# Kernel optimization log

Measured on AMD Instinct MI355X. Metric: run time of the kernel, lower is better.

The kernel has to match this reference:

```python
import jax, jax.numpy as jnp
import numpy as np

D = 128       # d_model
NHEAD = 4
R = 2         # n_rounds
CF = 32       # fine channels
H0, W0 = 40, 52
HF, WF = 160, 208
TEMP = 0.1
THR = 0.2
WIN = 5
STRIDE = 8


def setup_inputs() -> dict:
    key = jax.random.key(0)
    ks = jax.random.split(key, 24)
    s = 0.05
    f = jnp.float32
    n = lambda k, sh: jax.random.normal(k, sh, f)
    inp = {
        'coarse0': n(ks[0], (1, D, H0, W0)),
        'coarse1': n(ks[1], (1, D, H0, W0)),
        'fine0': n(ks[2], (1, CF, HF, WF)),
        'fine1': n(ks[3], (1, CF, HF, WF)),
        'sa_in_w': n(ks[4], (R, 3 * D, D)) * s,
        'sa_in_b': jnp.zeros((R, 3 * D), f),
        'sa_out_w': n(ks[5], (R, D, D)) * s,
        'sa_out_b': jnp.zeros((R, D), f),
        'ca_in_w': n(ks[6], (R, 3 * D, D)) * s,
        'ca_in_b': jnp.zeros((R, 3 * D), f),
        'ca_out_w': n(ks[7], (R, D, D)) * s,
        'ca_out_b': jnp.zeros((R, D), f),
        'sn_g': jnp.ones((R, D), f), 'sn_b': jnp.zeros((R, D), f),
        'cn_g': jnp.ones((R, D), f), 'cn_b': jnp.zeros((R, D), f),
        'ffn_w1': n(ks[8], (R, 2 * D, D)) * s,
        'ffn_b1': jnp.zeros((R, 2 * D), f),
        'ffn_w2': n(ks[9], (R, D, 2 * D)) * s,
        'ffn_b2': jnp.zeros((R, D), f),
        'fn_g': jnp.ones((R, D), f), 'fn_b': jnp.zeros((R, D), f),
        'proj_w': n(ks[10], (CF, CF)) * s,
        'proj_b': jnp.zeros((CF,), f),
    }
    return inp


def _ln(x, g, b):
    m = x.mean(-1, keepdims=True)
    v = ((x - m) ** 2).mean(-1, keepdims=True)
    return (x - m) * jax.lax.rsqrt(v + 1e-5) * g + b


def _mha(xq, xkv, in_w, in_b, out_w, out_b):
    B, Lq, d = xq.shape
    Lk = xkv.shape[1]
    h, dh = NHEAD, D // NHEAD
    q = (xq @ in_w[:d].T + in_b[:d]).reshape(B, Lq, h, dh)
    k = (xkv @ in_w[d:2 * d].T + in_b[d:2 * d]).reshape(B, Lk, h, dh)
    v = (xkv @ in_w[2 * d:].T + in_b[2 * d:]).reshape(B, Lk, h, dh)
    a = jnp.einsum('bqhd,bkhd->bhqk', q, k) / np.float32(np.sqrt(dh))
    a = jax.nn.softmax(a, axis=-1)
    o = jnp.einsum('bhqk,bkhd->bqhd', a, v).reshape(B, Lq, d)
    return o @ out_w.T + out_b


def _forward(coarse0, coarse1, fine0, fine1, sa_in_w, sa_in_b, sa_out_w, sa_out_b,
             ca_in_w, ca_in_b, ca_out_w, ca_out_b, sn_g, sn_b, cn_g, cn_b,
             ffn_w1, ffn_b1, ffn_w2, ffn_b2, fn_g, fn_b, proj_w, proj_b):
    B, C, H, W = coarse0.shape
    f0 = coarse0.reshape(B, C, H * W).transpose(0, 2, 1)
    f1 = coarse1.reshape(B, C, H * W).transpose(0, 2, 1)
    for i in range(R):
        f0 = _ln(f0 + _mha(f0, f0, sa_in_w[i], sa_in_b[i], sa_out_w[i], sa_out_b[i]), sn_g[i], sn_b[i])
        f1 = _ln(f1 + _mha(f1, f1, sa_in_w[i], sa_in_b[i], sa_out_w[i], sa_out_b[i]), sn_g[i], sn_b[i])
        f0c = _mha(f0, f1, ca_in_w[i], ca_in_b[i], ca_out_w[i], ca_out_b[i])
        f1c = _mha(f1, f0, ca_in_w[i], ca_in_b[i], ca_out_w[i], ca_out_b[i])
        f0 = _ln(f0 + f0c, cn_g[i], cn_b[i])
        f1 = _ln(f1 + f1c, cn_g[i], cn_b[i])
        f0 = _ln(f0 + jax.nn.relu(f0 @ ffn_w1[i].T + ffn_b1[i]) @ ffn_w2[i].T + ffn_b2[i], fn_g[i], fn_b[i])
        f1 = _ln(f1 + jax.nn.relu(f1 @ ffn_w1[i].T + ffn_b1[i]) @ ffn_w2[i].T + ffn_b2[i], fn_g[i], fn_b[i])
    # coarse matching: dual softmax + mutual NN
    f0n = f0 / jnp.maximum(jnp.linalg.norm(f0, axis=-1, keepdims=True), 1e-12)
    f1n = f1 / jnp.maximum(jnp.linalg.norm(f1, axis=-1, keepdims=True), 1e-12)
    S = jnp.einsum('bld,bmd->blm', f0n, f1n) / TEMP
    P = jax.nn.softmax(S, axis=-1) * jax.nn.softmax(S, axis=-2)
    P0 = P[0]
    L0 = H * W
    idx0 = jnp.argmax(P0, axis=-1)
    idx1 = jnp.argmax(P0, axis=0)
    conf = P0.max(axis=-1)
    valid = (idx1[idx0] == jnp.arange(L0)) & (conf > THR)
    ar = jnp.arange(L0)
    mk0 = jnp.stack([ar % W, ar // W], 1).astype(jnp.float32)
    mk1 = jnp.stack([idx0 % W, idx0 // W], 1).astype(jnp.float32)
    # fine refinement (vectorized over all L0 candidate matches)
    f0p = jnp.einsum('oc,chw->ohw', proj_w, fine0[0]) + proj_b[:, None, None]
    f1p = jnp.einsum('oc,chw->ohw', proj_w, fine1[0]) + proj_b[:, None, None]
    half = WIN // 2
    fr = STRIDE // 2
    c0 = (mk0 * fr).astype(jnp.int32)
    c1 = (mk1 * fr).astype(jnp.int32)
    Hf, Wf = f0p.shape[1], f0p.shape[2]
    inb = ((c0[:, 0] - half >= 0) & (c0[:, 0] + half < Wf) & (c0[:, 1] - half >= 0) & (c0[:, 1] + half < Hf)
           & (c1[:, 0] - half >= 0) & (c1[:, 0] + half < Wf) & (c1[:, 1] - half >= 0) & (c1[:, 1] + half < Hf))
    off = jnp.arange(WIN) - half
    cy0 = jnp.clip(c0[:, 1], half, Hf - 1 - half)
    cx0 = jnp.clip(c0[:, 0], half, Wf - 1 - half)
    cy1 = jnp.clip(c1[:, 1], half, Hf - 1 - half)
    cx1 = jnp.clip(c1[:, 0], half, Wf - 1 - half)
    center = f0p[:, cy0, cx0]                              # (C, N)
    y1 = cy1[:, None] + off
    x1 = cx1[:, None] + off
    patch1 = f1p[:, y1[:, :, None], x1[:, None, :]]
    corr = jnp.einsum('cn,cnhw->nhw', center, patch1)
    soft = jax.nn.softmax(corr.reshape(-1, WIN * WIN), axis=-1).reshape(-1, WIN, WIN)
    gx = off.astype(jnp.float32)[None, None, :]
    gy = off.astype(jnp.float32)[None, :, None]
    offx = (soft * gx).sum((1, 2))
    offy = (soft * gy).sum((1, 2))
    scale = np.float32(STRIDE // fr)
    pt0 = mk0 * STRIDE + STRIDE // 2
    base1 = mk1 * STRIDE + STRIDE // 2
    delta = jnp.stack([offx, offy], 1) * scale
    pt1 = base1 + jnp.where(inb[:, None], delta, 0.0)
    return P, valid, conf, pt0, pt1


def reference(coarse0, coarse1, fine0, fine1, sa_in_w, sa_in_b, sa_out_w, sa_out_b,
              ca_in_w, ca_in_b, ca_out_w, ca_out_b, sn_g, sn_b, cn_g, cn_b,
              ffn_w1, ffn_b1, ffn_w2, ffn_b2, fn_g, fn_b, proj_w, proj_b):
    return _forward(coarse0, coarse1, fine0, fine1, sa_in_w, sa_in_b, sa_out_w, sa_out_b,
                    ca_in_w, ca_in_b, ca_out_w, ca_out_b, sn_g, sn_b, cn_g, cn_b,
                    ffn_w1, ffn_b1, ffn_w2, ffn_b2, fn_g, fn_b, proj_w, proj_b)
```

## Files before the change

### kernel.cpp

```cpp
#include <hip/hip_runtime.h>
#include <math.h>

#define LTOK 2080
#define DIM 128
#define NH 4
#define W0C 52
#define HFI 160
#define WFI 208
#define NPIX (HFI*WFI)
#define CFCH 32
#define NSPLIT2 6
#define QBLK 64
#define NQB 33
#define PSTRIDE2 2112
#define NST 33

#define DOT4(q,k) ((q).x*(k).x + (q).y*(k).y + (q).z*(k).z + (q).w*(k).w)

__global__ __launch_bounds__(256) void transpose_b_kernel(const float* __restrict__ in0,
                                                          const float* __restrict__ in1,
                                                          float* __restrict__ out0,
                                                          float* __restrict__ out1)
{
    const float* in = blockIdx.z ? in1 : in0;
    float* out = blockIdx.z ? out1 : out0;
    __shared__ float T[32][33];
    int l0 = blockIdx.x * 32, c0 = blockIdx.y * 32;
    int t = threadIdx.x;
    #pragma unroll
    for (int e = 0; e < 4; ++e) {
        int idx = t + e * 256; int i = idx >> 5, j = idx & 31;
        T[i][j] = in[(size_t)(c0 + i) * LTOK + l0 + j];
    }
    __syncthreads();
    #pragma unroll
    for (int e = 0; e < 4; ++e) {
        int idx = t + e * 256; int j2 = idx >> 5, i2 = idx & 31;
        out[(size_t)(l0 + j2) * DIM + c0 + i2] = T[i2][j2];
    }
}

__global__ __launch_bounds__(256) void gemm64_nt_b2_kernel(const float* __restrict__ A0,
                                                           const float* __restrict__ A1, int lda,
                                                           const float* __restrict__ B, int ldb,
                                                           float* __restrict__ C0,
                                                           float* __restrict__ C1, int ldc,
                                                           int K,
                                                           const float* __restrict__ bias, int relu,
                                                           int M)
{
    const float* A = blockIdx.z ? A1 : A0;
    float* C = blockIdx.z ? C1 : C0;
    __shared__ float As[32][68];
    __shared__ float Bs[32][68];
    int tid = threadIdx.x;
    int n0 = blockIdx.x * 64, m0 = blockIdx.y * 64;
    int cg = tid & 15, rg = tid >> 4;
    int r0 = rg * 4, c0 = cg * 4;
    int srow = tid & 63;
    int skq  = tid >> 6;
    float4 acc0 = make_float4(0.f,0.f,0.f,0.f);
    float4 acc1 = make_float4(0.f,0.f,0.f,0.f);
    float4 acc2 = make_float4(0.f,0.f,0.f,0.f);
    float4 acc3 = make_float4(0.f,0.f,0.f,0.f);

    for (int k0 = 0; k0 < K; k0 += 32) {
        int ar = m0 + srow; ar = ar < M ? ar : M - 1;
        int br = n0 + srow;
        const float* ap = A + (size_t)ar * lda + k0 + skq * 8;
        const float* bp = B + (size_t)br * ldb + k0 + skq * 8;
        float4 av0 = *(const float4*)(ap);
        float4 av1 = *(const float4*)(ap + 4);
        float4 bv0 = *(const float4*)(bp);
        float4 bv1 = *(const float4*)(bp + 4);
        int kk = skq * 8;
        As[kk+0][srow] = av0.x; As[kk+1][srow] = av0.y; As[kk+2][srow] = av0.z; As[kk+3][srow] = av0.w;
        As[kk+4][srow] = av1.x; As[kk+5][srow] = av1.y; As[kk+6][srow] = av1.z; As[kk+7][srow] = av1.w;
        Bs[kk+0][srow] = bv0.x; Bs[kk+1][srow] = bv0.y; Bs[kk+2][srow] = bv0.z; Bs[kk+3][srow] = bv0.w;
        Bs[kk+4][srow] = bv1.x; Bs[kk+5][srow] = bv1.y; Bs[kk+6][srow] = bv1.z; Bs[kk+7][srow] = bv1.w;
        __syncthreads();
        #pragma unroll
        for (int k = 0; k < 32; ++k) {
            float4 a = *(const float4*)(&As[k][r0]);
            float4 b = *(const float4*)(&Bs[k][c0]);
            acc0.x += a.x*b.x; acc0.y += a.x*b.y; acc0.z += a.x*b.z; acc0.w += a.x*b.w;
            acc1.x += a.y*b.x; acc1.y += a.y*b.y; acc1.z += a.y*b.z; acc1.w += a.y*b.w;
            acc2.x += a.z*b.x; acc2.y += a.z*b.y; acc2.z += a.z*b.z; acc2.w += a.z*b.w;
            acc3.x += a.w*b.x; acc3.y += a.w*b.y; acc3.z += a.w*b.z; acc3.w += a.w*b.w;
        }
        __syncthreads();
    }
    float4 bv = make_float4(0.f,0.f,0.f,0.f);
    if (bias) bv = *(const float4*)(bias + n0 + c0);
    acc0.x += bv.x; acc0.y += bv.y; acc0.z += bv.z; acc0.w += bv.w;
    acc1.x += bv.x; acc1.y += bv.y; acc1.z += bv.z; acc1.w += bv.w;
    acc2.x += bv.x; acc2.y += bv.y; acc2.z += bv.z; acc2.w += bv.w;
    acc3.x += bv.x; acc3.y += bv.y; acc3.z += bv.z; acc3.w += bv.w;
    if (relu) {
        acc0.x = fmaxf(acc0.x, 0.f); acc0.y = fmaxf(acc0.y, 0.f); acc0.z = fmaxf(acc0.z, 0.f); acc0.w = fmaxf(acc0.w, 0.f);
        acc1.x = fmaxf(acc1.x, 0.f); acc1.y = fmaxf(acc1.y, 0.f); acc1.z = fmaxf(acc1.z, 0.f); acc1.w = fmaxf(acc1.w, 0.f);
        acc2.x = fmaxf(acc2.x, 0.f); acc2.y = fmaxf(acc2.y, 0.f); acc2.z = fmaxf(acc2.z, 0.f); acc2.w = fmaxf(acc2.w, 0.f);
        acc3.x = fmaxf(acc3.x, 0.f); acc3.y = fmaxf(acc3.y, 0.f); acc3.z = fmaxf(acc3.z, 0.f); acc3.w = fmaxf(acc3.w, 0.f);
    }
    int gr = m0 + r0;
    if (gr + 0 < M) *(float4*)(C + (size_t)(gr + 0) * ldc + n0 + c0) = acc0;
    if (gr + 1 < M) *(float4*)(C + (size_t)(gr + 1) * ldc + n0 + c0) = acc1;
    if (gr + 2 < M) *(float4*)(C + (size_t)(gr + 2) * ldc + n0 + c0) = acc2;
    if (gr + 3 < M) *(float4*)(C + (size_t)(gr + 3) * ldc + n0 + c0) = acc3;
}

__global__ __launch_bounds__(256) void gemm_score64_kernel(const float* __restrict__ A,
                                                           const float* __restrict__ B,
                                                           float* __restrict__ C,
                                                           float2* __restrict__ prs,
                                                           float2* __restrict__ pcs)
{
    __shared__ float As[32][68];
    __shared__ float Bs[32][68];
    __shared__ float cmS[16][68];
    __shared__ float ceS[16][68];
    int tid = threadIdx.x;
    int n0 = blockIdx.x * 64, m0 = blockIdx.y * 64;
    int cg = tid & 15, rg = tid >> 4;
    int r0 = rg * 4, c0 = cg * 4;
    int srow = tid & 63;
    int skq  = tid >> 6;
    float4 acc0 = make_float4(0.f,0.f,0.f,0.f);
    float4 acc1 = make_float4(0.f,0.f,0.f,0.f);
    float4 acc2 = make_float4(0.f,0.f,0.f,0.f);
    float4 acc3 = make_float4(0.f,0.f,0.f,0.f);

    for (int k0 = 0; k0 < 128; k0 += 32) {
        int ar = m0 + srow; ar = ar < LTOK ? ar : LTOK - 1;
        int br = n0 + srow; br = br < LTOK ? br : LTOK - 1;
        const float* ap = A + (size_t)ar * 128 + k0 + skq * 8;
        const float* bp = B + (size_t)br * 128 + k0 + skq * 8;
        float4 av0 = *(const float4*)(ap);
        float4 av1 = *(const float4*)(ap + 4);
        float4 bv0 = *(const float4*)(bp);
        float4 bv1 = *(const float4*)(bp + 4);
        int kk = skq * 8;
        As[kk+0][srow] = av0.x; As[kk+1][srow] = av0.y; As[kk+2][srow] = av0.z; As[kk+3][srow] = av0.w;
        As[kk+4][srow] = av1.x; As[kk+5][srow] = av1.y; As[kk+6][srow] = av1.z; As[kk+7][srow] = av1.w;
        Bs[kk+0][srow] = bv0.x; Bs[kk+1][srow] = bv0.y; Bs[kk+2][srow] = bv0.z; Bs[kk+3][srow] = bv0.w;
        Bs[kk+4][srow] = bv1.x; Bs[kk+5][srow] = bv1.y; Bs[kk+6][srow] = bv1.z; Bs[kk+7][srow] = bv1.w;
        __syncthreads();
        #pragma unroll
        for (int k = 0; k < 32; ++k) {
            float4 a = *(const float4*)(&As[k][r0]);
            float4 b = *(const float4*)(&Bs[k][c0]);
            acc0.x += a.x*b.x; acc0.y += a.x*b.y; acc0.z += a.x*b.z; acc0.w += a.x*b.w;
            acc1.x += a.y*b.x; acc1.y += a.y*b.y; acc1.z += a.y*b.z; acc1.w += a.y*b.w;
            acc2.x += a.z*b.x; acc2.y += a.z*b.y; acc2.z += a.z*b.z; acc2.w += a.z*b.w;
            acc3.x += a.w*b.x; acc3.y += a.w*b.y; acc3.z += a.w*b.z; acc3.w += a.w*b.w;
        }
        __syncthreads();
    }
    acc0.x *= 10.f; acc0.y *= 10.f; acc0.z *= 10.f; acc0.w *= 10.f;
    acc1.x *= 10.f; acc1.y *= 10.f; acc1.z *= 10.f; acc1.w *= 10.f;
    acc2.x *= 10.f; acc2.y *= 10.f; acc2.z *= 10.f; acc2.w *= 10.f;
    acc3.x *= 10.f; acc3.y *= 10.f; acc3.z *= 10.f; acc3.w *= 10.f;
    int gr = m0 + r0;
    bool colv = (n0 + c0) < LTOK;
    if (colv) {
        if (gr + 0 < LTOK) *(float4*)(C + (size_t)(gr + 0) * LTOK + n0 + c0) = acc0;
        if (gr + 1 < LTOK) *(float4*)(C + (size_t)(gr + 1) * LTOK + n0 + c0) = acc1;
        if (gr + 2 < LTOK) *(float4*)(C + (size_t)(gr + 2) * LTOK + n0 + c0) = acc2;
        if (gr + 3 < LTOK) *(float4*)(C + (size_t)(gr + 3) * LTOK + n0 + c0) = acc3;
    }
    const float NEG = -1e30f;
    float v00 = colv ? acc0.x : NEG, v01 = colv ? acc0.y : NEG, v02 = colv ? acc0.z : NEG, v03 = colv ? acc0.w : NEG;
    float v10 = colv ? acc1.x : NEG, v11 = colv ? acc1.y : NEG, v12 = colv ? acc1.z : NEG, v13 = colv ? acc1.w : NEG;
    float v20 = colv ? acc2.x : NEG, v21 = colv ? acc2.y : NEG, v22 = colv ? acc2.z : NEG, v23 = colv ? acc2.w : NEG;
    float v30 = colv ? acc3.x : NEG, v31 = colv ? acc3.y : NEG, v32 = colv ? acc3.z : NEG, v33 = colv ? acc3.w : NEG;
    #pragma unroll
    for (int i = 0; i < 4; ++i) {
        float a = (i==0)?v00:(i==1)?v10:(i==2)?v20:v30;
        float b = (i==0)?v01:(i==1)?v11:(i==2)?v21:v31;
        float c = (i==0)?v02:(i==1)?v12:(i==2)?v22:v32;
        float d = (i==0)?v03:(i==1)?v13:(i==2)?v23:v33;
        float m = fmaxf(fmaxf(a,b), fmaxf(c,d));
        float e = 0.f;
        if (m > NEG) e = __expf(a-m) + __expf(b-m) + __expf(c-m) + __expf(d-m);
        #pragma unroll
        for (int mm = 8; mm >= 1; mm >>= 1) {
            float m2 = __shfl_xor(m, mm, 16);
            float e2 = __shfl_xor(e, mm, 16);
            if (m2 > m) { e = e * __expf(m - m2) + e2; m = m2; }
            else if (m2 > NEG) { e += e2 * __expf(m2 - m); }
        }
        if (cg == 0 && gr + i < LTOK)
            prs[(size_t)blockIdx.x * LTOK + gr + i] = make_float2(m, e);
    }
    bool rv0 = (gr + 0) < LTOK, rv1 = (gr + 1) < LTOK, rv2 = (gr + 2) < LTOK, rv3 = (gr + 3) < LTOK;
    #pragma unroll
    for (int j = 0; j < 4; ++j) {
        float a = rv0 ? ((j==0)?v00:(j==1)?v01:(j==2)?v02:v03) : NEG;
        float b = rv1 ? ((j==0)?v10:(j==1)?v11:(j==2)?v12:v13) : NEG;
        float c = rv2 ? ((j==0)?v20:(j==1)?v21:(j==2)?v22:v23) : NEG;
        float d = rv3 ? ((j==0)?v30:(j==1)?v31:(j==2)?v32:v33) : NEG;
        float m = fmaxf(fmaxf(a,b), fmaxf(c,d));
        float e = 0.f;
        if (m > NEG) {
            if (rv0) e += __expf(a-m);
            if (rv1) e += __expf(b-m);
            if (rv2) e += __expf(c-m);
            if (rv3) e += __expf(d-m);
        }
        cmS[rg][c0 + j] = m;
        ceS[rg][c0 + j] = e;
    }
    __syncthreads();
    if (tid < 64) {
        int col = tid;
        float m = cmS[0][col], e = ceS[0][col];
        #pragma unroll
        for (int k = 1; k < 16; ++k) {
            float m2 = cmS[k][col], e2 = ceS[k][col];
            if (m2 > m) { e = e * __expf(m - m2) + e2; m = m2; }
            else if (m2 > NEG) { e += e2 * __expf(m2 - m); }
        }
        if (n0 + col < LTOK)
            pcs[(size_t)blockIdx.y * LTOK + n0 + col] = make_float2(m, e);
    }
}

__global__ __launch_bounds__(256) void stats_combine_kernel(const float2* __restrict__ prs,
                                                            const float2* __restrict__ pcs,
                                                            float* __restrict__ rowmax,
                                                            float* __restrict__ rsinv,
                                                            float* __restrict__ colmax,
                                                            float* __restrict__ csinv)
{
    int id = blockIdx.x * 256 + threadIdx.x;
    if (id >= 2 * LTOK) return;
    const float2* p = (id < LTOK) ? (prs + id) : (pcs + (id - LTOK));
    float M = -1e30f;
    for (int i = 0; i < NST; ++i) M = fmaxf(M, p[(size_t)i * LTOK].x);
    float S = 0.f;
    for (int i = 0; i < NST; ++i) {
        float2 f = p[(size_t)i * LTOK];
        S += f.y * __expf(f.x - M);
    }
    if (id < LTOK) { rowmax[id] = M; rsinv[id] = 1.f / S; }
    else           { colmax[id - LTOK] = M; csinv[id - LTOK] = 1.f / S; }
}

__global__ __launch_bounds__(256) void dualp_argmax_kernel(float* __restrict__ S,
                                                           const float* __restrict__ rm,
                                                           const float* __restrict__ rsinv,
                                                           const float* __restrict__ cm,
                                                           const float* __restrict__ csinv,
                                                           float* __restrict__ prv,
                                                           int* __restrict__ pri,
                                                           float* __restrict__ pcv,
                                                           int* __restrict__ pci)
{
    __shared__ float cvS[8][32];
    __shared__ int   ciS[8][32];
    int tid = threadIdx.x;
    int n0 = blockIdx.x * 32, m0 = blockIdx.y * 32;
    int c = tid & 31, r8 = tid >> 5;
    int col = n0 + c;
    float cmv = cm[col], csv = csinv[col];
    float p[4];
    #pragma unroll
    for (int jj = 0; jj < 4; ++jj) {
        int row = m0 + 4 * r8 + jj;
        size_t o = (size_t)row * LTOK + col;
        float s = S[o];
        float pv = __expf(2.f * s - rm[row] - cmv) * (rsinv[row] * csv);
        S[o] = pv;
        p[jj] = pv;
    }
    #pragma unroll
    for (int jj = 0; jj < 4; ++jj) {
        float bv = p[jj]; int bi = col;
        #pragma unroll
        for (int mm = 16; mm >= 1; mm >>= 1) {
            float ov = __shfl_xor(bv, mm, 32);
            int   oi = __shfl_xor(bi, mm, 32);
            if (ov > bv || (ov == bv && oi < bi)) { bv = ov; bi = oi; }
        }
        if (c == 0) {
            prv[(size_t)blockIdx.x * LTOK + m0 + 4 * r8 + jj] = bv;
            pri[(size_t)blockIdx.x * LTOK + m0 + 4 * r8 + jj] = bi;
        }
    }
    float bv = p[0]; int bi = m0 + 4 * r8;
    #pragma unroll
    for (int jj = 1; jj < 4; ++jj)
        if (p[jj] > bv) { bv = p[jj]; bi = m0 + 4 * r8 + jj; }
    cvS[r8][c] = bv; ciS[r8][c] = bi;
    __syncthreads();
    if (r8 == 0) {
        #pragma unroll
        for (int k = 1; k < 8; ++k)
            if (cvS[k][c] > bv) { bv = cvS[k][c]; bi = ciS[k][c]; }
        pcv[(size_t)blockIdx.y * LTOK + col] = bv;
        pci[(size_t)blockIdx.y * LTOK + col] = bi;
    }
}

__global__ __launch_bounds__(256) void argmax_combine_kernel(const float* __restrict__ prv,
                                                             const int* __restrict__ pri,
                                                             const float* __restrict__ pcv,
                                                             const int* __restrict__ pci,
                                                             int* __restrict__ idx0,
                                                             float* __restrict__ conf,
                                                             int* __restrict__ idx1)
{
    int id = blockIdx.x * 256 + threadIdx.x;
    if (id >= 2 * LTOK) return;
    if (id < LTOK) {
        float best = -1e30f; int bi = 0;
        for (int i = 0; i < 65; ++i) {
            float v = prv[(size_t)i * LTOK + id];
            if (v > best) { best = v; bi = pri[(size_t)i * LTOK + id]; }
        }
        idx0[id] = bi; conf[id] = best;
    } else {
        int colI = id - LTOK;
        float best = -1e30f; int bi = 0;
        for (int i = 0; i < 65; ++i) {
            float v = pcv[(size_t)i * LTOK + colI];
            if (v > best) { best = v; bi = pci[(size_t)i * LTOK + colI]; }
        }
        idx1[colI] = bi;
    }
}

__global__ __launch_bounds__(256, 3) void mha_partial2_kernel(const float* __restrict__ qkvA,
                                                              const float* __restrict__ qkvB,
                                                              int cross,
                                                              float* __restrict__ part)
{
    __shared__ float Qs[QBLK][36];
    __shared__ float Ks[64][36];
    __shared__ float Vt[32][68];
    __shared__ float Ps[QBLK][68];
    int tid = threadIdx.x;
    int qb = blockIdx.x, ns = blockIdx.z;
    int img = blockIdx.y >> 2, h = blockIdx.y & 3;
    const float* qsrc  = img ? qkvB : qkvA;
    const float* kvsrc = cross ? (img ? qkvA : qkvB) : qsrc;
    int c4 = tid & 15;
    int rg = tid >> 4;
    const int r0 = rg * 4;
    const float sc = 0.17677669529663687f;

    {
        int r = tid >> 2, d8 = (tid & 3) << 3;
        int qr = qb * QBLK + r; qr = qr < LTOK ? qr : (LTOK - 1);
        const float* src = qsrc + (size_t)qr * 384 + h * 32 + d8;
        *(float4*)(&Qs[r][d8])     = *(const float4*)(src);
        *(float4*)(&Qs[r][d8 + 4]) = *(const float4*)(src + 4);
    }
    float a00=0.f,a01=0.f,a10=0.f,a11=0.f,a20=0.f,a21=0.f,a30=0.f,a31=0.f;
    float l0=0.f,l1=0.f,l2=0.f,l3=0.f;
    __syncthreads();

    const int koff = 128 + h * 32, voff = 256 + h * 32;
    for (int t = ns; t < 33; t += NSPLIT2) {
        int j0 = t * 64;
        {
            int r = tid >> 3, d4 = (tid & 7) << 2;
            int j1 = j0 + r, j2 = j0 + r + 32;
            float4 k1 = *(const float4*)(kvsrc + (size_t)j1 * 384 + koff + d4);
            float4 v1 = *(const float4*)(kvsrc + (size_t)j1 * 384 + voff + d4);
            float4 k2 = make_float4(0.f, 0.f, 0.f, 0.f);
            float4 v2 = make_float4(0.f, 0.f, 0.f, 0.f);
            if (j2 < LTOK) {
                k2 = *(const float4*)(kvsrc + (size_t)j2 * 384 + koff + d4);
                v2 = *(const float4*)(kvsrc + (size_t)j2 * 384 + voff + d4);
            }
            *(float4*)(&Ks[r][d4])      = k1;
            *(float4*)(&Ks[r + 32][d4]) = k2;
            Vt[d4 + 0][r] = v1.x; Vt[d4 + 1][r] = v1.y; Vt[d4 + 2][r] = v1.z; Vt[d4 + 3][r] = v1.w;
            Vt[d4 + 0][r + 32] = v2.x; Vt[d4 + 1][r + 32] = v2.y; Vt[d4 + 2][r + 32] = v2.z; Vt[d4 + 3][r + 32] = v2.w;
        }
        __syncthreads();
        float s00=0.f,s01=0.f,s02=0.f,s03=0.f;
        float s10=0.f,s11=0.f,s12=0.f,s13=0.f;
        float s20=0.f,s21=0.f,s22=0.f,s23=0.f;
        float s30=0.f,s31=0.f,s32=0.f,s33=0.f;
        #pragma unroll
        for (int d4 = 0; d4 < 8; ++d4) {
            const int db = d4 << 2;
            float4 k0 = *(const float4*)(&Ks[c4][db]);
            float4 k1 = *(const float4*)(&Ks[c4 + 16][db]);
            float4 k2 = *(const float4*)(&Ks[c4 + 32][db]);
            float4 k3 = *(const float4*)(&Ks[c4 + 48][db]);
            float4 q0 = *(const float4*)(&Qs[r0 + 0][db]);
            float4 q1 = *(const float4*)(&Qs[r0 + 1][db]);
            float4 q2 = *(const float4*)(&Qs[r0 + 2][db]);
            float4 q3 = *(const float4*)(&Qs[r0 + 3][db]);
            s00 += DOT4(q0,k0); s01 += DOT4(q0,k1); s02 += DOT4(q0,k2); s03 += DOT4(q0,k3);
            s10 += DOT4(q1,k0); s11 += DOT4(q1,k1); s12 += DOT4(q1,k2); s13 += DOT4(q1,k3);
            s20 += DOT4(q2,k0); s21 += DOT4(q2,k1); s22 += DOT4(q2,k2); s23 += DOT4(q2,k3);
            s30 += DOT4(q3,k0); s31 += DOT4(q3,k1); s32 += DOT4(q3,k2); s33 += DOT4(q3,k3);
        }
        bool ok0 = (j0 + c4) < LTOK;
        bool ok1 = (j0 + 16 + c4) < LTOK;
        bool ok2 = (j0 + 32 + c4) < LTOK;
        bool ok3 = (j0 + 48 + c4) < LTOK;
        {
            float p0 = ok0 ? __expf(s00 * sc) : 0.f;
            float p1 = ok1 ? __expf(s01 * sc) : 0.f;
            float p2 = ok2 ? __expf(s02 * sc) : 0.f;
            float p3 = ok3 ? __expf(s03 * sc) : 0.f;
            l0 += p0 + p1 + p2 + p3;
            Ps[r0 + 0][c4] = p0; Ps[r0 + 0][c4 + 16] = p1; Ps[r0 + 0][c4 + 32] = p2; Ps[r0 + 0][c4 + 48] = p3;
        }
        {
            float p0 = ok0 ? __expf(s10 * sc) : 0.f;
            float p1 = ok1 ? __expf(s11 * sc) : 0.f;
            float p2 = ok2 ? __expf(s12 * sc) : 0.f;
            float p3 = ok3 ? __expf(s13 * sc) : 0.f;
            l1 += p0 + p1 + p2 + p3;
            Ps[r0 + 1][c4] = p0; Ps[r0 + 1][c4 + 16] = p1; Ps[r0 + 1][c4 + 32] = p2; Ps[r0 + 1][c4 + 48] = p3;
        }
        {
            float p0 = ok0 ? __expf(s20 * sc) : 0.f;
            float p1 = ok1 ? __expf(s21 * sc) : 0.f;
            float p2 = ok2 ? __expf(s22 * sc) : 0.f;
            float p3 = ok3 ? __expf(s23 * sc) : 0.f;
            l2 += p0 + p1 + p2 + p3;
            Ps[r0 + 2][c4] = p0; Ps[r0 + 2][c4 + 16] = p1; Ps[r0 + 2][c4 + 32] = p2; Ps[r0 + 2][c4 + 48] = p3;
        }
        {
            float p0 = ok0 ? __expf(s30 * sc) : 0.f;
            float p1 = ok1 ? __expf(s31 * sc) : 0.f;
            float p2 = ok2 ? __expf(s32 * sc) : 0.f;
            float p3 = ok3 ? __expf(s33 * sc) : 0.f;
            l3 += p0 + p1 + p2 + p3;
            Ps[r0 + 3][c4] = p0; Ps[r0 + 3][c4 + 16] = p1; Ps[r0 + 3][c4 + 32] = p2; Ps[r0 + 3][c4 + 48] = p3;
        }
        __syncthreads();
        #pragma unroll
        for (int j4 = 0; j4 < 16; ++j4) {
            const int jb = j4 << 2;
            float4 v0 = *(const float4*)(&Vt[c4][jb]);
            float4 v1 = *(const float4*)(&Vt[c4 + 16][jb]);
            float4 pq0 = *(const float4*)(&Ps[r0 + 0][jb]);
            float4 pq1 = *(const float4*)(&Ps[r0 + 1][jb]);
            float4 pq2 = *(const float4*)(&Ps[r0 + 2][jb]);
            float4 pq3 = *(const float4*)(&Ps[r0 + 3][jb]);
            a00 += DOT4(pq0,v0); a01 += DOT4(pq0,v1);
            a10 += DOT4(pq1,v0); a11 += DOT4(pq1,v1);
            a20 += DOT4(pq2,v0); a21 += DOT4(pq2,v1);
            a30 += DOT4(pq3,v0); a31 += DOT4(pq3,v1);
        }
        __syncthreads();
    }
    float* pb = part + (size_t)((((size_t)img * NQB + qb) * NH + h) * NSPLIT2 + ns) * PSTRIDE2;
    pb[(r0 + 0) * 32 + c4]      = a00;
    pb[(r0 + 0) * 32 + c4 + 16] = a01;
    pb[(r0 + 1) * 32 + c4]      = a10;
    pb[(r0 + 1) * 32 + c4 + 16] = a11;
    pb[(r0 + 2) * 32 + c4]      = a20;
    pb[(r0 + 2) * 32 + c4 + 16] = a21;
    pb[(r0 + 3) * 32 + c4]      = a30;
    pb[(r0 + 3) * 32 + c4 + 16] = a31;
    #pragma unroll
    for (int mm = 8; mm >= 1; mm >>= 1) {
        l0 += __shfl_xor(l0, mm, 16);
        l1 += __shfl_xor(l1, mm, 16);
        l2 += __shfl_xor(l2, mm, 16);
        l3 += __shfl_xor(l3, mm, 16);
    }
    if (c4 == 0) {
        pb[2048 + r0 + 0] = l0;
        pb[2048 + r0 + 1] = l1;
        pb[2048 + r0 + 2] = l2;
        pb[2048 + r0 + 3] = l3;
    }
}

__global__ __launch_bounds__(256) void mha_combine2_kernel(const float* __restrict__ part,
                                                           float* __restrict__ out0,
                                                           float* __restrict__ out1)
{
    int tid = threadIdx.x;
    int qb = blockIdx.x;
    int img = blockIdx.y >> 2, h = blockIdx.y & 3;
    float* out = img ? out1 : out0;
    int c = tid & 31, rg8 = tid >> 5;
    const float* pb = part + (size_t)(((size_t)img * NQB + qb) * NH + h) * NSPLIT2 * PSTRIDE2;
    #pragma unroll
    for (int jj = 0; jj < 8; ++jj) {
        int row = rg8 * 8 + jj;
        int qrow = qb * QBLK + row;
        if (qrow >= LTOK) continue;
        float num = 0.f, den = 0.f;
        #pragma unroll
        for (int ns = 0; ns < NSPLIT2; ++ns) {
            num += pb[ns * PSTRIDE2 + row * 32 + c];
            den += pb[ns * PSTRIDE2 + 2048 + row];
        }
        out[(size_t)qrow * DIM + h * 32 + c] = num / den;
    }
}

__global__ __launch_bounds__(256) void addln_b_kernel(float* __restrict__ f0,
                                                      float* __restrict__ f1,
                                                      const float* __restrict__ t0,
                                                      const float* __restrict__ t1,
                                                      const float* __restrict__ g,
                                                      const float* __restrict__ b)
{
    float* f = blockIdx.y ? f1 : f0;
    const float* t = blockIdx.y ? t1 : t0;
    int row = blockIdx.x * 4 + (threadIdx.x >> 6);
    int lane = threadIdx.x & 63;
    size_t base = (size_t)row * DIM;
    float x0 = f[base + lane] + t[base + lane];
    float x1 = f[base + lane + 64] + t[base + lane + 64];
    float s = x0 + x1;
    #pragma unroll
    for (int mm = 32; mm >= 1; mm >>= 1) s += __shfl_xor(s, mm, 64);
    float mean = s * (1.f / 128.f);
    float d0 = x0 - mean, d1 = x1 - mean;
    float v = d0 * d0 + d1 * d1;
    #pragma unroll
    for (int mm = 32; mm >= 1; mm >>= 1) v += __shfl_xor(v, mm, 64);
    float rstd = rsqrtf(v * (1.f / 128.f) + 1e-5f);
    f[base + lane]      = d0 * rstd * g[lane] + b[lane];
    f[base + lane + 64] = d1 * rstd * g[lane + 64] + b[lane + 64];
}

__global__ __launch_bounds__(256) void normrows_b_kernel(const float* __restrict__ i0,
                                                         const float* __restrict__ i1,
                                                         float* __restrict__ o0,
                                                         float* __restrict__ o1)
{
    const float* f = blockIdx.y ? i1 : i0;
    float* o = blockIdx.y ? o1 : o0;
    int row = blockIdx.x * 4 + (threadIdx.x >> 6);
    int lane = threadIdx.x & 63;
    size_t base = (size_t)row * DIM;
    float x0 = f[base + lane], x1 = f[base + lane + 64];
    float v = x0 * x0 + x1 * x1;
    #pragma unroll
    for (int mm = 32; mm >= 1; mm >>= 1) v += __shfl_xor(v, mm, 64);
    float inv = 1.f / fmaxf(sqrtf(v), 1e-12f);
    o[base + lane] = x0 * inv;
    o[base + lane + 64] = x1 * inv;
}

__global__ __launch_bounds__(256) void match_kernel(const int* __restrict__ idx0,
                                                    const int* __restrict__ idx1,
                                                    const float* __restrict__ conf,
                                                    float* __restrict__ out_valid,
                                                    float* __restrict__ out_conf,
                                                    float* __restrict__ out_pt0)
{
    int i = blockIdx.x * 256 + threadIdx.x;
    if (i >= LTOK) return;
    int j = idx0[i];
    bool valid = (idx1[j] == i) && (conf[i] > 0.2f);
    out_valid[i] = valid ? 1.f : 0.f;
    out_conf[i] = conf[i];
    out_pt0[2 * i]     = (float)(i % W0C) * 8.f + 4.f;
    out_pt0[2 * i + 1] = (float)(i / W0C) * 8.f + 4.f;
}

__global__ __launch_bounds__(256) void fine_proj_b_kernel(const float* __restrict__ fin0,
                                                          const float* __restrict__ fin1,
                                                          const float* __restrict__ w,
                                                          const float* __restrict__ b,
                                                          float* __restrict__ fout0,
                                                          float* __restrict__ fout1)
{
    const float* fin = blockIdx.y ? fin1 : fin0;
    float* fout = blockIdx.y ? fout1 : fout0;
    __shared__ float ws_[32][32];
    __shared__ float bs[32];
    int t = threadIdx.x;
    #pragma unroll
    for (int e = 0; e < 4; ++e) { int l = t + e * 256; ws_[l >> 5][l & 31] = w[l]; }
    if (t < 32) bs[t] = b[t];
    __syncthreads();
    int p = blockIdx.x * 256 + t;
    if (p >= NPIX) return;
    float x[32];
    #pragma unroll
    for (int cc = 0; cc < 32; ++cc) x[cc] = fin[(size_t)cc * NPIX + p];
    #pragma unroll
    for (int o = 0; o < 32; ++o) {
        float a = bs[o];
        #pragma unroll
        for (int cc = 0; cc < 32; ++cc) a += ws_[o][cc] * x[cc];
        fout[(size_t)o * NPIX + p] = a;
    }
}

__global__ __launch_bounds__(64) void fine_match_kernel(const int* __restrict__ idx0,
                                                        const float* __restrict__ f0p,
                                                        const float* __restrict__ f1p,
                                                        float* __restrict__ out_pt1)
{
    int i = blockIdx.x;
    int l = threadIdx.x;
    int j = idx0[i];
    int m0x = i % W0C, m0y = i / W0C;
    int m1x = j % W0C, m1y = j / W0C;
    int c0x = m0x * 4, c0y = m0y * 4, c1x = m1x * 4, c1y = m1y * 4;
    bool inb = (c0x - 2 >= 0) && (c0x + 2 < WFI) && (c0y - 2 >= 0) && (c0y + 2 < HFI)
            && (c1x - 2 >= 0) && (c1x + 2 < WFI) && (c1y - 2 >= 0) && (c1y + 2 < HFI);
    int cy0 = min(max(c0y, 2), HFI - 3), cx0 = min(max(c0x, 2), WFI - 3);
    int cy1 = min(max(c1y, 2), HFI - 3), cx1 = min(max(c1x, 2), WFI - 3);
    int dy = l / 5 - 2, dx = l % 5 - 2;
    float corr = -1e30f;
    if (l < 25) {
        float a = 0.f;
        int p0 = cy0 * WFI + cx0;
        int p1 = (cy1 + dy) * WFI + (cx1 + dx);
        #pragma unroll
        for (int cc = 0; cc < 32; ++cc)
            a += f0p[(size_t)cc * NPIX + p0] * f1p[(size_t)cc * NPIX + p1];
        corr = a;
    }
    float mx = corr;
    #pragma unroll
    for (int mm = 32; mm >= 1; mm >>= 1) mx = fmaxf(mx, __shfl_xor(mx, mm, 64));
    float p = (l < 25) ? expf(corr - mx) : 0.f;
    float s = p, sx = p * (float)dx, sy = p * (float)dy;
    #pragma unroll
    for (int mm = 32; mm >= 1; mm >>= 1) {
        s  += __shfl_xor(s, mm, 64);
        sx += __shfl_xor(sx, mm, 64);
        sy += __shfl_xor(sy, mm, 64);
    }
    if (l == 0) {
        float offx = sx / s, offy = sy / s;
        float px = (float)m1x * 8.f + 4.f;
        float py = (float)m1y * 8.f + 4.f;
        if (inb) { px += offx * 2.f; py += offy * 2.f; }
        out_pt1[2 * i]     = px;
        out_pt1[2 * i + 1] = py;
    }
}

extern "C" void kernel_launch(void* const* d_in, const int* in_sizes, int n_in,
                              void* d_out, int out_size, void* d_ws, size_t ws_size,
                              hipStream_t stream) {
    (void)in_sizes; (void)n_in; (void)out_size; (void)ws_size;
    const float* coarse0 = (const float*)d_in[0];
    const float* coarse1 = (const float*)d_in[1];
    const float* fine0   = (const float*)d_in[2];
    const float* fine1   = (const float*)d_in[3];
    const float* sa_in_w  = (const float*)d_in[4];
    const float* sa_in_b  = (const float*)d_in[5];
    const float* sa_out_w = (const float*)d_in[6];
    const float* sa_out_b = (const float*)d_in[7];
    const float* ca_in_w  = (const float*)d_in[8];
    const float* ca_in_b  = (const float*)d_in[9];
    const float* ca_out_w = (const float*)d_in[10];
    const float* ca_out_b = (const float*)d_in[11];
    const float* sn_g = (const float*)d_in[12];
    const float* sn_b = (const float*)d_in[13];
    const float* cn_g = (const float*)d_in[14];
    const float* cn_b = (const float*)d_in[15];
    const float* ffn_w1 = (const float*)d_in[16];
    const float* ffn_b1 = (const float*)d_in[17];
    const float* ffn_w2 = (const float*)d_in[18];
    const float* ffn_b2 = (const float*)d_in[19];
    const float* fn_g = (const float*)d_in[20];
    const float* fn_b = (const float*)d_in[21];
    const float* proj_w = (const float*)d_in[22];
    const float* proj_b = (const float*)d_in[23];

    float* w = (float*)d_ws;
    float* f0   = w; w += (size_t)LTOK * DIM;
    float* f1   = w; w += (size_t)LTOK * DIM;
    float* qkv0 = w; w += (size_t)LTOK * 384;
    float* qkv1 = w; w += (size_t)LTOK * 384;
    float* att0 = w; w += (size_t)LTOK * DIM;
    float* att1 = w; w += (size_t)LTOK * DIM;
    float* tmp0 = w; w += (size_t)LTOK * DIM;
    float* tmp1 = w; w += (size_t)LTOK * DIM;
    float* f0n  = w; w += (size_t)LTOK * DIM;
    float* f1n  = w; w += (size_t)LTOK * DIM;
    float* R1   = w; w += (size_t)3345408;
    float* rowmax = w; w += LTOK;
    float* rsinv  = w; w += LTOK;
    float* colmax = w; w += LTOK;
    float* csinv  = w; w += LTOK;
    float* conf   = w; w += LTOK;
    int* idx0 = (int*)w; w += LTOK;
    int* idx1 = (int*)w; w += LTOK;

    float* part = R1;
    float* hid0 = R1;
    float* hid1 = R1 + (size_t)LTOK * 256;
    float* f0p  = R1;
    float* f1p  = R1 + (size_t)CFCH * NPIX;

    float2* prs = (float2*)qkv0;
    float2* pcs = (float2*)(qkv0 + 2 * NST * LTOK);
    float*  prv = qkv1;
    int*    pri = (int*)(qkv1 + 65 * LTOK);
    float*  pcv = qkv1 + 2 * 65 * LTOK;
    int*    pci = (int*)(qkv1 + 3 * 65 * LTOK);

    float* Pout = (float*)d_out;
    float* out_valid = Pout + (size_t)LTOK * LTOK;
    float* out_conf  = out_valid + LTOK;
    float* out_pt0   = out_conf + LTOK;
    float* out_pt1   = out_pt0 + 2 * LTOK;

    dim3 b256(256);
    dim3 gMHA(NQB, 8, NSPLIT2);
    dim3 gCMB(NQB, 8);
    dim3 gLN(520, 2);
    transpose_b_kernel<<<dim3(65, 4, 2), b256, 0, stream>>>(coarse0, coarse1, f0, f1);

    for (int i = 0; i < 2; ++i) {
        const float* saw = sa_in_w + (size_t)i * 384 * 128;
        const float* sab = sa_in_b + (size_t)i * 384;
        const float* sow = sa_out_w + (size_t)i * 128 * 128;
        const float* sob = sa_out_b + (size_t)i * 128;
        const float* caw = ca_in_w + (size_t)i * 384 * 128;
        const float* cab = ca_in_b + (size_t)i * 384;
        const float* cow = ca_out_w + (size_t)i * 128 * 128;
        const float* cob = ca_out_b + (size_t)i * 128;
        const float* w1 = ffn_w1 + (size_t)i * 256 * 128;
        const float* b1 = ffn_b1 + (size_t)i * 256;
        const float* w2 = ffn_w2 + (size_t)i * 128 * 256;
        const float* b2 = ffn_b2 + (size_t)i * 128;

        gemm64_nt_b2_kernel<<<dim3(6, 33, 2), b256, 0, stream>>>(f0, f1, 128, saw, 128, qkv0, qkv1, 384, 128, sab, 0, LTOK);
        mha_partial2_kernel<<<gMHA, b256, 0, stream>>>(qkv0, qkv1, 0, part);
        mha_combine2_kernel<<<gCMB, b256, 0, stream>>>(part, att0, att1);
        gemm64_nt_b2_kernel<<<dim3(2, 33, 2), b256, 0, stream>>>(att0, att1, 128, sow, 128, tmp0, tmp1, 128, 128, sob, 0, LTOK);
        addln_b_kernel<<<gLN, b256, 0, stream>>>(f0, f1, tmp0, tmp1, sn_g + (size_t)i * 128, sn_b + (size_t)i * 128);

        gemm64_nt_b2_kernel<<<dim3(6, 33, 2), b256, 0, stream>>>(f0, f1, 128, caw, 128, qkv0, qkv1, 384, 128, cab, 0, LTOK);
        mha_partial2_kernel<<<gMHA, b256, 0, stream>>>(qkv0, qkv1, 1, part);
        mha_combine2_kernel<<<gCMB, b256, 0, stream>>>(part, att0, att1);
        gemm64_nt_b2_kernel<<<dim3(2, 33, 2), b256, 0, stream>>>(att0, att1, 128, cow, 128, tmp0, tmp1, 128, 128, cob, 0, LTOK);
        addln_b_kernel<<<gLN, b256, 0, stream>>>(f0, f1, tmp0, tmp1, cn_g + (size_t)i * 128, cn_b + (size_t)i * 128);

        gemm64_nt_b2_kernel<<<dim3(4, 33, 2), b256, 0, stream>>>(f0, f1, 128, w1, 128, hid0, hid1, 256, 128, b1, 1, LTOK);
        gemm64_nt_b2_kernel<<<dim3(2, 33, 2), b256, 0, stream>>>(hid0, hid1, 256, w2, 256, tmp0, tmp1, 128, 256, b2, 0, LTOK);
        addln_b_kernel<<<gLN, b256, 0, stream>>>(f0, f1, tmp0, tmp1, fn_g + (size_t)i * 128, fn_b + (size_t)i * 128);
    }

    normrows_b_kernel<<<gLN, b256, 0, stream>>>(f0, f1, f0n, f1n);
    gemm_score64_kernel<<<dim3(NST, NST), b256, 0, stream>>>(f0n, f1n, Pout, prs, pcs);
    stats_combine_kernel<<<17, b256, 0, stream>>>(prs, pcs, rowmax, rsinv, colmax, csinv);
    dualp_argmax_kernel<<<dim3(65, 65), b256, 0, stream>>>(Pout, rowmax, rsinv, colmax, csinv,
                                                           prv, pri, pcv, pci);
    argmax_combine_kernel<<<17, b256, 0, stream>>>(prv, pri, pcv, pci, idx0, conf, idx1);
    match_kernel<<<9, b256, 0, stream>>>(idx0, idx1, conf, out_valid, out_conf, out_pt0);

    fine_proj_b_kernel<<<dim3(130, 2), b256, 0, stream>>>(fine0, fine1, proj_w, proj_b, f0p, f1p);
    fine_match_kernel<<<LTOK, dim3(64), 0, stream>>>(idx0, f0p, f1p, out_pt1);
}
```

Measured before the change: 783.6 us.

## Fuse attention combine, output projection, residual add and LayerNorm into one kernel

```diff
diff --git a/kernel.cpp b/kernel.cpp
--- a/kernel.cpp
+++ b/kernel.cpp
@@ -107,6 +107,143 @@
     if (gr + 1 < M) *(float4*)(C + (size_t)(gr + 1) * ldc + n0 + c0) = acc1;
     if (gr + 2 < M) *(float4*)(C + (size_t)(gr + 2) * ldc + n0 + c0) = acc2;
     if (gr + 3 < M) *(float4*)(C + (size_t)(gr + 3) * ldc + n0 + c0) = acc3;
+}
+
+#define LNROW(AA, AB, I)                                                                \
+    {                                                                                   \
+        int row = gr + (I); bool ok = row < LTOK;                                       \
+        const float* fr = F + (size_t)(ok ? row : 0) * DIM;                             \
+        float4 f0v = *(const float4*)(fr + c0);                                         \
+        float4 f1v = *(const float4*)(fr + c0 + 64);                                    \
+        float x0x = AA.x + bb0.x + f0v.x, x0y = AA.y + bb0.y + f0v.y;                   \
+        float x0z = AA.z + bb0.z + f0v.z, x0w = AA.w + bb0.w + f0v.w;                   \
+        float x1x = AB.x + bb1.x + f1v.x, x1y = AB.y + bb1.y + f1v.y;                   \
+        float x1z = AB.z + bb1.z + f1v.z, x1w = AB.w + bb1.w + f1v.w;                   \
+        float s = x0x + x0y + x0z + x0w + x1x + x1y + x1z + x1w;                        \
+        s += __shfl_xor(s, 8, 16); s += __shfl_xor(s, 4, 16);                           \
+        s += __shfl_xor(s, 2, 16); s += __shfl_xor(s, 1, 16);                           \
+        float mean = s * (1.f / 128.f);                                                 \
+        float d0x = x0x - mean, d0y = x0y - mean, d0z = x0z - mean, d0w = x0w - mean;   \
+        float d1x = x1x - mean, d1y = x1y - mean, d1z = x1z - mean, d1w = x1w - mean;   \
+        float vv = d0x*d0x + d0y*d0y + d0z*d0z + d0w*d0w                                \
+                 + d1x*d1x + d1y*d1y + d1z*d1z + d1w*d1w;                               \
+        vv += __shfl_xor(vv, 8, 16); vv += __shfl_xor(vv, 4, 16);                       \
+        vv += __shfl_xor(vv, 2, 16); vv += __shfl_xor(vv, 1, 16);                       \
+        float rstd = rsqrtf(vv * (1.f / 128.f) + 1e-5f);                                \
+        if (ok) {                                                                       \
+            float4 o0, o1;                                                              \
+            o0.x = d0x * rstd * g0.x + be0.x; o0.y = d0y * rstd * g0.y + be0.y;         \
+            o0.z = d0z * rstd * g0.z + be0.z; o0.w = d0w * rstd * g0.w + be0.w;         \
+            o1.x = d1x * rstd * g1.x + be1.x; o1.y = d1y * rstd * g1.y + be1.y;         \
+            o1.z = d1z * rstd * g1.z + be1.z; o1.w = d1w * rstd * g1.w + be1.w;         \
+            *(float4*)(F + (size_t)row * DIM + c0) = o0;                                \
+            *(float4*)(F + (size_t)row * DIM + c0 + 64) = o1;                           \
+        }                                                                               \
+    }
+
+__global__ __launch_bounds__(256) void gemm128_ln_kernel(const float* __restrict__ A0,
+                                                         const float* __restrict__ A1, int lda,
+                                                         int K, int mode,
+                                                         const float* __restrict__ part,
+                                                         const float* __restrict__ B, int ldb,
+                                                         const float* __restrict__ bias,
+                                                         const float* __restrict__ g,
+                                                         const float* __restrict__ bvec,
+                                                         float* __restrict__ F0,
+                                                         float* __restrict__ F1)
+{
+    __shared__ float As[32][68];
+    __shared__ float Bs[32][132];
+    __shared__ float denS[4][64];
+    int tid = threadIdx.x;
+    int qb = blockIdx.x, img = blockIdx.y;
+    const float* A = img ? A1 : A0;
+    float* F = img ? F1 : F0;
+    int m0 = qb * 64;
+    int cg = tid & 15, rg = tid >> 4;
+    int r0 = rg * 4, c0 = cg * 4;
+    int srow = tid & 63, skq = tid >> 6;
+
+    if (mode) {
+        int h = tid >> 6, row = tid & 63;
+        const float* pb = part + ((((size_t)img * NQB + qb) * NH + h) * NSPLIT2) * PSTRIDE2;
+        float dd = 0.f;
+        #pragma unroll
+        for (int ns = 0; ns < NSPLIT2; ++ns) dd += pb[ns * PSTRIDE2 + 2048 + row];
+        denS[h][row] = dd;
+        __syncthreads();
+    }
+
+    float4 aA0 = make_float4(0.f,0.f,0.f,0.f), aB0 = aA0;
+    float4 aA1 = aA0, aB1 = aA0, aA2 = aA0, aB2 = aA0, aA3 = aA0, aB3 = aA0;
+
+    for (int k0 = 0; k0 < K; k0 += 32) {
+        int kk = skq * 8;
+        if (mode) {
+            const float* pb = part + ((((size_t)img * NQB + qb) * NH + (k0 >> 5)) * NSPLIT2) * PSTRIDE2
+                              + srow * 32 + kk;
+            float n0x=0.f,n0y=0.f,n0z=0.f,n0w=0.f,n1x=0.f,n1y=0.f,n1z=0.f,n1w=0.f;
+            #pragma unroll
+            for (int ns = 0; ns < NSPLIT2; ++ns) {
+                float4 u0 = *(const float4*)(pb + ns * PSTRIDE2);
+                float4 u1 = *(const float4*)(pb + ns * PSTRIDE2 + 4);
+                n0x += u0.x; n0y += u0.y; n0z += u0.z; n0w += u0.w;
+                n1x += u1.x; n1y += u1.y; n1z += u1.z; n1w += u1.w;
+            }
+            float dd = denS[k0 >> 5][srow];
+            As[kk+0][srow] = n0x / dd; As[kk+1][srow] = n0y / dd;
+            As[kk+2][srow] = n0z / dd; As[kk+3][srow] = n0w / dd;
+            As[kk+4][srow] = n1x / dd; As[kk+5][srow] = n1y / dd;
+            As[kk+6][srow] = n1z / dd; As[kk+7][srow] = n1w / dd;
+        } else {
+            int ar = m0 + srow; ar = ar < LTOK ? ar : LTOK - 1;
+            const float* ap = A + (size_t)ar * lda + k0 + kk;
+            float4 av0 = *(const float4*)(ap);
+            float4 av1 = *(const float4*)(ap + 4);
+            As[kk+0][srow] = av0.x; As[kk+1][srow] = av0.y; As[kk+2][srow] = av0.z; As[kk+3][srow] = av0.w;
+            As[kk+4][srow] = av1.x; As[kk+5][srow] = av1.y; As[kk+6][srow] = av1.z; As[kk+7][srow] = av1.w;
+        }
+        {
+            int n = tid & 127, kh = tid >> 7;
+            const float* bp = B + (size_t)n * ldb + k0 + kh * 16;
+            float4 b0 = *(const float4*)(bp);
+            float4 b1 = *(const float4*)(bp + 4);
+            float4 b2 = *(const float4*)(bp + 8);
+            float4 b3 = *(const float4*)(bp + 12);
+            int kb = kh * 16;
+            Bs[kb+ 0][n] = b0.x; Bs[kb+ 1][n] = b0.y; Bs[kb+ 2][n] = b0.z; Bs[kb+ 3][n] = b0.w;
+            Bs[kb+ 4][n] = b1.x; Bs[kb+ 5][n] = b1.y; Bs[kb+ 6][n] = b1.z; Bs[kb+ 7][n] = b1.w;
+            Bs[kb+ 8][n] = b2.x; Bs[kb+ 9][n] = b2.y; Bs[kb+10][n] = b2.z; Bs[kb+11][n] = b2.w;
+            Bs[kb+12][n] = b3.x; Bs[kb+13][n] = b3.y; Bs[kb+14][n] = b3.z; Bs[kb+15][n] = b3.w;
+        }
+        __syncthreads();
+        #pragma unroll
+        for (int k = 0; k < 32; ++k) {
+            float4 a  = *(const float4*)(&As[k][r0]);
+            float4 b0 = *(const float4*)(&Bs[k][c0]);
+            float4 b1 = *(const float4*)(&Bs[k][c0 + 64]);
+            aA0.x += a.x*b0.x; aA0.y += a.x*b0.y; aA0.z += a.x*b0.z; aA0.w += a.x*b0.w;
+            aB0.x += a.x*b1.x; aB0.y += a.x*b1.y; aB0.z += a.x*b1.z; aB0.w += a.x*b1.w;
+            aA1.x += a.y*b0.x; aA1.y += a.y*b0.y; aA1.z += a.y*b0.z; aA1.w += a.y*b0.w;
+            aB1.x += a.y*b1.x; aB1.y += a.y*b1.y; aB1.z += a.y*b1.z; aB1.w += a.y*b1.w;
+            aA2.x += a.z*b0.x; aA2.y += a.z*b0.y; aA2.z += a.z*b0.z; aA2.w += a.z*b0.w;
+            aB2.x += a.z*b1.x; aB2.y += a.z*b1.y; aB2.z += a.z*b1.z; aB2.w += a.z*b1.w;
+            aA3.x += a.w*b0.x; aA3.y += a.w*b0.y; aA3.z += a.w*b0.z; aA3.w += a.w*b0.w;
+            aB3.x += a.w*b1.x; aB3.y += a.w*b1.y; aB3.z += a.w*b1.z; aB3.w += a.w*b1.w;
+        }
+        __syncthreads();
+    }
+    float4 bb0 = *(const float4*)(bias + c0);
+    float4 bb1 = *(const float4*)(bias + c0 + 64);
+    float4 g0  = *(const float4*)(g + c0);
+    float4 g1  = *(const float4*)(g + c0 + 64);
+    float4 be0 = *(const float4*)(bvec + c0);
+    float4 be1 = *(const float4*)(bvec + c0 + 64);
+    int gr = m0 + r0;
+    LNROW(aA0, aB0, 0)
+    LNROW(aA1, aB1, 1)
+    LNROW(aA2, aB2, 2)
+    LNROW(aA3, aB3, 3)
 }
 
 __global__ __launch_bounds__(256) void gemm_score64_kernel(const float* __restrict__ A,
@@ -475,58 +612,6 @@
         pb[2048 + r0 + 2] = l2;
         pb[2048 + r0 + 3] = l3;
     }
-}
-
-__global__ __launch_bounds__(256) void mha_combine2_kernel(const float* __restrict__ part,
-                                                           float* __restrict__ out0,
-                                                           float* __restrict__ out1)
-{
-    int tid = threadIdx.x;
-    int qb = blockIdx.x;
-    int img = blockIdx.y >> 2, h = blockIdx.y & 3;
-    float* out = img ? out1 : out0;
-    int c = tid & 31, rg8 = tid >> 5;
-    const float* pb = part + (size_t)(((size_t)img * NQB + qb) * NH + h) * NSPLIT2 * PSTRIDE2;
-    #pragma unroll
-    for (int jj = 0; jj < 8; ++jj) {
-        int row = rg8 * 8 + jj;
-        int qrow = qb * QBLK + row;
-        if (qrow >= LTOK) continue;
-        float num = 0.f, den = 0.f;
-        #pragma unroll
-        for (int ns = 0; ns < NSPLIT2; ++ns) {
-            num += pb[ns * PSTRIDE2 + row * 32 + c];
-            den += pb[ns * PSTRIDE2 + 2048 + row];
-        }
-        out[(size_t)qrow * DIM + h * 32 + c] = num / den;
-    }
-}
-
-__global__ __launch_bounds__(256) void addln_b_kernel(float* __restrict__ f0,
-                                                      float* __restrict__ f1,
-                                                      const float* __restrict__ t0,
-                                                      const float* __restrict__ t1,
-                                                      const float* __restrict__ g,
-                                                      const float* __restrict__ b)
-{
-    float* f = blockIdx.y ? f1 : f0;
-    const float* t = blockIdx.y ? t1 : t0;
-    int row = blockIdx.x * 4 + (threadIdx.x >> 6);
-    int lane = threadIdx.x & 63;
-    size_t base = (size_t)row * DIM;
-    float x0 = f[base + lane] + t[base + lane];
-    float x1 = f[base + lane + 64] + t[base + lane + 64];
-    float s = x0 + x1;
-    #pragma unroll
-    for (int mm = 32; mm >= 1; mm >>= 1) s += __shfl_xor(s, mm, 64);
-    float mean = s * (1.f / 128.f);
-    float d0 = x0 - mean, d1 = x1 - mean;
-    float v = d0 * d0 + d1 * d1;
-    #pragma unroll
-    for (int mm = 32; mm >= 1; mm >>= 1) v += __shfl_xor(v, mm, 64);
-    float rstd = rsqrtf(v * (1.f / 128.f) + 1e-5f);
-    f[base + lane]      = d0 * rstd * g[lane] + b[lane];
-    f[base + lane + 64] = d1 * rstd * g[lane + 64] + b[lane + 64];
 }
 
 __global__ __launch_bounds__(256) void normrows_b_kernel(const float* __restrict__ i0,
@@ -676,10 +761,6 @@
     float* f1   = w; w += (size_t)LTOK * DIM;
     float* qkv0 = w; w += (size_t)LTOK * 384;
     float* qkv1 = w; w += (size_t)LTOK * 384;
-    float* att0 = w; w += (size_t)LTOK * DIM;
-    float* att1 = w; w += (size_t)LTOK * DIM;
-    float* tmp0 = w; w += (size_t)LTOK * DIM;
-    float* tmp1 = w; w += (size_t)LTOK * DIM;
     float* f0n  = w; w += (size_t)LTOK * DIM;
     float* f1n  = w; w += (size_t)LTOK * DIM;
     float* R1   = w; w += (size_t)3345408;
@@ -712,7 +793,7 @@
 
     dim3 b256(256);
     dim3 gMHA(NQB, 8, NSPLIT2);
-    dim3 gCMB(NQB, 8);
+    dim3 gFLN(NQB, 2);
     dim3 gLN(520, 2);
     transpose_b_kernel<<<dim3(65, 4, 2), b256, 0, stream>>>(coarse0, coarse1, f0, f1);
 
@@ -732,19 +813,23 @@
 
         gemm64_nt_b2_kernel<<<dim3(6, 33, 2), b256, 0, stream>>>(f0, f1, 128, saw, 128, qkv0, qkv1, 384, 128, sab, 0, LTOK);
         mha_partial2_kernel<<<gMHA, b256, 0, stream>>>(qkv0, qkv1, 0, part);
-        mha_combine2_kernel<<<gCMB, b256, 0, stream>>>(part, att0, att1);
-        gemm64_nt_b2_kernel<<<dim3(2, 33, 2), b256, 0, stream>>>(att0, att1, 128, sow, 128, tmp0, tmp1, 128, 128, sob, 0, LTOK);
-        addln_b_kernel<<<gLN, b256, 0, stream>>>(f0, f1, tmp0, tmp1, sn_g + (size_t)i * 128, sn_b + (size_t)i * 128);
+        gemm128_ln_kernel<<<gFLN, b256, 0, stream>>>(nullptr, nullptr, 0, 128, 1, part,
+                                                     sow, 128, sob,
+                                                     sn_g + (size_t)i * 128, sn_b + (size_t)i * 128,
+                                                     f0, f1);
 
         gemm64_nt_b2_kernel<<<dim3(6, 33, 2), b256, 0, stream>>>(f0, f1, 128, caw, 128, qkv0, qkv1, 384, 128, cab, 0, LTOK);
         mha_partial2_kernel<<<gMHA, b256, 0, stream>>>(qkv0, qkv1, 1, part);
-        mha_combine2_kernel<<<gCMB, b256, 0, stream>>>(part, att0, att1);
-        gemm64_nt_b2_kernel<<<dim3(2, 33, 2), b256, 0, stream>>>(att0, att1, 128, cow, 128, tmp0, tmp1, 128, 128, cob, 0, LTOK);
-        addln_b_kernel<<<gLN, b256, 0, stream>>>(f0, f1, tmp0, tmp1, cn_g + (size_t)i * 128, cn_b + (size_t)i * 128);
+        gemm128_ln_kernel<<<gFLN, b256, 0, stream>>>(nullptr, nullptr, 0, 128, 1, part,
+                                                     cow, 128, cob,
+                                                     cn_g + (size_t)i * 128, cn_b + (size_t)i * 128,
+                                                     f0, f1);
 
         gemm64_nt_b2_kernel<<<dim3(4, 33, 2), b256, 0, stream>>>(f0, f1, 128, w1, 128, hid0, hid1, 256, 128, b1, 1, LTOK);
-        gemm64_nt_b2_kernel<<<dim3(2, 33, 2), b256, 0, stream>>>(hid0, hid1, 256, w2, 256, tmp0, tmp1, 128, 256, b2, 0, LTOK);
-        addln_b_kernel<<<gLN, b256, 0, stream>>>(f0, f1, tmp0, tmp1, fn_g + (size_t)i * 128, fn_b + (size_t)i * 128);
+        gemm128_ln_kernel<<<gFLN, b256, 0, stream>>>(hid0, hid1, 256, 256, 0, nullptr,
+                                                     w2, 256, b2,
+                                                     fn_g + (size_t)i * 128, fn_b + (size_t)i * 128,
+                                                     f0, f1);
     }
 
     normrows_b_kernel<<<gLN, b256, 0, stream>>>(f0, f1, f0n, f1n);
```

Result: no change. 794.6 us (+1.4%).
